# Performance work log

Hardware: AMD Instinct MI355X
Metric: run time of the kernel (lower is better)

The kernel has to match this reference:

```python
import jax, jax.numpy as jnp
import numpy as np

NUM_HEADS = 16

def _apply_rope(x, cos, sin):
    # x: (B, H, T, D); cos/sin: (T, D//2)
    B, H, T, D = x.shape
    xr = x.reshape(B, H, T, D // 2, 2)
    x0, x1 = xr[..., 0], xr[..., 1]
    c = cos[None, None, :, :]
    s = sin[None, None, :, :]
    out = jnp.stack([x0 * c - x1 * s, x0 * s + x1 * c], axis=-1)
    return out.reshape(B, H, T, D)


def setup_inputs() -> dict:
    key = jax.random.key(0)
    k1, k2, k3 = jax.random.split(key, 3)
    B, T, C = 2, 2048, 1024
    D = C // NUM_HEADS
    x = jax.random.normal(k1, (B, T, C), dtype=jnp.float32)
    qkv_w = jax.random.normal(k2, (3 * C, C), dtype=jnp.float32) * (C ** -0.5)
    proj_w = jax.random.normal(k3, (C, C), dtype=jnp.float32) * (C ** -0.5)
    # standard RoPE frequency table (theta = 10000)
    inv_freq = 1.0 / (10000.0 ** (jnp.arange(0, D, 2, dtype=jnp.float32) / D))  # (D/2,)
    angles = jnp.arange(T, dtype=jnp.float32)[:, None] * inv_freq[None, :]      # (T, D/2)
    return {
        "x": x,
        "freqs_cos": jnp.cos(angles),
        "freqs_sin": jnp.sin(angles),
        "qkv_w": qkv_w,
        "proj_w": proj_w,
    }


def reference(x, freqs_cos, freqs_sin, qkv_w, proj_w):
    B, T, C = x.shape
    H = NUM_HEADS
    D = C // H
    qkv = x @ qkv_w.T                                  # (B, T, 3C)
    q, k, v = jnp.split(qkv, 3, axis=-1)
    q = q.reshape(B, T, H, D).transpose(0, 2, 1, 3)    # (B, H, T, D)
    k = k.reshape(B, T, H, D).transpose(0, 2, 1, 3)
    v = v.reshape(B, T, H, D).transpose(0, 2, 1, 3)
    q = _apply_rope(q, freqs_cos, freqs_sin)
    k = _apply_rope(k, freqs_cos, freqs_sin)
    scale = 1.0 / jnp.sqrt(jnp.asarray(D, dtype=x.dtype))
    scores = jnp.einsum('bhqd,bhkd->bhqk', q, k) * scale
    causal = jnp.tril(jnp.ones((T, T), dtype=bool))
    scores = jnp.where(causal[None, None], scores, jnp.finfo(scores.dtype).min)
    attn = jax.nn.softmax(scores, axis=-1)
    out = jnp.einsum('bhqk,bhkd->bhqd', attn, v)       # (B, H, T, D)
    out = out.transpose(0, 2, 1, 3).reshape(B, T, C)
    return out @ proj_w.T
```

## Files before the change

### kernel.cpp

```cpp
#include <hip/hip_runtime.h>
#include <stdint.h>

#define DI __device__ __forceinline__

typedef unsigned short u16;
typedef __bf16 bf16x8 __attribute__((ext_vector_type(8)));
typedef unsigned short u16x8 __attribute__((ext_vector_type(8)));
typedef unsigned short u16x4 __attribute__((ext_vector_type(4)));
typedef float f32x4 __attribute__((ext_vector_type(4)));

DI u16 f2bf(float f) { __bf16 h = (__bf16)f; return __builtin_bit_cast(u16, h); }
DI float bf2f(u16 u) { return (float)__builtin_bit_cast(__bf16, u); }

DI bf16x8 ld8(const u16* p) { return __builtin_bit_cast(bf16x8, *(const u16x8*)p); }

DI f32x4 mfma16(bf16x8 a, bf16x8 b, f32x4 c) {
  return __builtin_amdgcn_mfma_f32_16x16x32_bf16(a, b, c, 0, 0, 0);
}

DI void async16(const u16* g, u16* l) {
  __builtin_amdgcn_global_load_lds((const __attribute__((address_space(1))) void*)g,
                                   (__attribute__((address_space(3))) void*)l, 16, 0, 0);
}

__global__ __launch_bounds__(256) void cast_bf16_k(const float* __restrict__ in,
                                                   u16* __restrict__ out) {
  const int i = blockIdx.x * 256 + threadIdx.x;
  const float4 v = ((const float4*)in)[i];
  u16x4 o = {f2bf(v.x), f2bf(v.y), f2bf(v.z), f2bf(v.w)};
  ((u16x4*)out)[i] = o;
}

template <int OUT_BF16>
__global__ __launch_bounds__(256) void gemm_bt(const u16* __restrict__ A,
                                               const u16* __restrict__ W,
                                               void* __restrict__ outp,
                                               int M, int N, int K) {
  __shared__ u16 sA[128 * 32];
  __shared__ u16 sB[128 * 32];
  const int tid = threadIdx.x;
  const int w = tid >> 6, L = tid & 63;
  const int lo = L & 15, quad = L >> 4;
  const int nb = N >> 7;
  const int bm = blockIdx.x / nb, bn = blockIdx.x - bm * nb;
  const int m0 = bm << 7, n0 = bn << 7;
  const int wm = (w >> 1) << 6, wn = (w & 1) << 6;

  f32x4 acc[4][4];
#pragma unroll
  for (int i = 0; i < 4; ++i)
#pragma unroll
    for (int j = 0; j < 4; ++j) acc[i][j] = 0.f;

  const int r0 = tid >> 2, s0 = tid & 3;
  const int c0 = s0 ^ ((r0 >> 1) & 3);
  const int r1 = r0 + 64;
  const int c1 = s0 ^ ((r1 >> 1) & 3);
  const size_t aRow0 = (size_t)(m0 + r0) * K, aRow1 = (size_t)(m0 + r1) * K;
  const size_t bRow0 = (size_t)(n0 + r0) * K, bRow1 = (size_t)(n0 + r1) * K;

  int raf[4], rbf[4];
#pragma unroll
  for (int mt = 0; mt < 4; ++mt) {
    int r = wm + mt * 16 + lo;
    raf[mt] = r * 32 + ((quad ^ ((r >> 1) & 3)) << 3);
    r = wn + mt * 16 + lo;
    rbf[mt] = r * 32 + ((quad ^ ((r >> 1) & 3)) << 3);
  }

  const int kIters = K >> 5;
  for (int kt = 0; kt < kIters; ++kt) {
    const int kb = kt << 5;
    async16(A + aRow0 + kb + c0 * 8, &sA[tid * 8]);
    async16(A + aRow1 + kb + c1 * 8, &sA[(tid + 256) * 8]);
    async16(W + bRow0 + kb + c0 * 8, &sB[tid * 8]);
    async16(W + bRow1 + kb + c1 * 8, &sB[(tid + 256) * 8]);
    __syncthreads();
    bf16x8 af[4], bfr[4];
#pragma unroll
    for (int mt = 0; mt < 4; ++mt) af[mt] = ld8(&sA[raf[mt]]);
#pragma unroll
    for (int nt = 0; nt < 4; ++nt) bfr[nt] = ld8(&sB[rbf[nt]]);
#pragma unroll
    for (int mt = 0; mt < 4; ++mt)
#pragma unroll
      for (int nt = 0; nt < 4; ++nt)
        acc[mt][nt] = mfma16(af[mt], bfr[nt], acc[mt][nt]);
    __syncthreads();
  }

#pragma unroll
  for (int mt = 0; mt < 4; ++mt) {
    const int m = m0 + wm + mt * 16 + quad * 4;
#pragma unroll
    for (int nt = 0; nt < 4; ++nt) {
      const int n = n0 + wn + nt * 16 + lo;
#pragma unroll
      for (int r = 0; r < 4; ++r) {
        const size_t off = (size_t)(m + r) * N + n;
        if (OUT_BF16)
          ((u16*)outp)[off] = f2bf(acc[mt][nt][r]);
        else
          ((float*)outp)[off] = acc[mt][nt][r];
      }
    }
  }
}

__global__ __launch_bounds__(256) void rope_k(const u16* __restrict__ qkv,
                                              const float* __restrict__ cosb,
                                              const float* __restrict__ sinb,
                                              u16* __restrict__ qo, u16* __restrict__ ko,
                                              u16* __restrict__ vo) {
  const int idx = blockIdx.x * 256 + threadIdx.x;
  const int i = idx & 31;
  const int t = (idx >> 5) & 2047;
  const int h = (idx >> 16) & 15;
  const int b = idx >> 20;
  const size_t src = ((size_t)(b * 2048 + t)) * 3072 + h * 64 + 2 * i;
  const float q0v = bf2f(qkv[src]), q1v = bf2f(qkv[src + 1]);
  const float k0v = bf2f(qkv[src + 1024]), k1v = bf2f(qkv[src + 1025]);
  const float c = cosb[t * 32 + i], s = sinb[t * 32 + i];
  const size_t dst = ((size_t)((b * 16 + h) * 2048 + t)) * 64 + 2 * i;
  qo[dst] = f2bf((q0v * c - q1v * s) * 0.125f);
  qo[dst + 1] = f2bf((q0v * s + q1v * c) * 0.125f);
  ko[dst] = f2bf(k0v * c - k1v * s);
  ko[dst + 1] = f2bf(k0v * s + k1v * c);
  vo[dst] = qkv[src + 2048];
  vo[dst + 1] = qkv[src + 2049];
}

__global__ __launch_bounds__(256) void fattn(const u16* __restrict__ qs,
                                             const u16* __restrict__ ks,
                                             const u16* __restrict__ vs,
                                             u16* __restrict__ aout) {
  __shared__ u16 sK[64 * 64];
  __shared__ u16 sVt[64 * 64];
  __shared__ u16 sP[4][32 * 64];
  const int tid = threadIdx.x;
  const int w = tid >> 6, L = tid & 63;
  const int lo = L & 15, quad = L >> 4;
  const int bh = blockIdx.x & 31;
  const int qi = 15 - (blockIdx.x >> 5);
  const size_t hoff = (size_t)bh * (2048 * 64);
  const int q0 = qi << 7;
  const int wq = q0 + w * 32;
  u16* sPw = sP[w];

  bf16x8 qb[2][2];
#pragma unroll
  for (int nt = 0; nt < 2; ++nt)
#pragma unroll
    for (int kd = 0; kd < 2; ++kd)
      qb[nt][kd] = ld8(qs + hoff + (size_t)(wq + nt * 16 + lo) * 64 + kd * 32 + quad * 8);

  float m_s[2] = {-3.0e38f, -3.0e38f};
  float l_s[2] = {0.f, 0.f};
  f32x4 ot[4][2];
#pragma unroll
  for (int mt = 0; mt < 4; ++mt) {
    ot[mt][0] = 0.f;
    ot[mt][1] = 0.f;
  }

  const int ntiles = (q0 + 128) >> 6;
  for (int kt = 0; kt < ntiles; ++kt) {
    const int kv0 = kt << 6;
#pragma unroll
    for (int it = 0; it < 2; ++it) {
      const int id = tid + it * 256;
      const int kv = id >> 3, s = id & 7, c = s ^ (kv & 7);
      async16(ks + hoff + (size_t)(kv0 + kv) * 64 + c * 8, &sK[id * 8]);
    }
#pragma unroll
    for (int it = 0; it < 2; ++it) {
      const int id = tid + it * 256;
      const int kv = id & 63, cd = id >> 6;
      u16x8 v8 = *(const u16x8*)(vs + hoff + (size_t)(kv0 + kv) * 64 + cd * 8);
#pragma unroll
      for (int j = 0; j < 8; ++j) {
        const int d = cd * 8 + j;
        sVt[d * 64 + (((kv >> 3) ^ (d & 7)) << 3) + (kv & 7)] = v8[j];
      }
    }
    __syncthreads();
    if (kv0 <= wq + 31) {
      f32x4 st[4][2];
#pragma unroll
      for (int mt = 0; mt < 4; ++mt) {
        st[mt][0] = 0.f;
        st[mt][1] = 0.f;
      }
#pragma unroll
      for (int mt = 0; mt < 4; ++mt) {
        const int kv = mt * 16 + lo;
#pragma unroll
        for (int kd = 0; kd < 2; ++kd) {
          const int c = kd * 4 + quad;
          bf16x8 ka = ld8(&sK[kv * 64 + ((c ^ (kv & 7)) << 3)]);
          st[mt][0] = mfma16(ka, qb[0][kd], st[mt][0]);
          st[mt][1] = mfma16(ka, qb[1][kd], st[mt][1]);
        }
      }
      if (kv0 + 63 > wq) {
#pragma unroll
        for (int mt = 0; mt < 4; ++mt)
#pragma unroll
          for (int nt = 0; nt < 2; ++nt)
#pragma unroll
            for (int r = 0; r < 4; ++r) {
              const int kvg = kv0 + mt * 16 + quad * 4 + r;
              const int qg = wq + nt * 16 + lo;
              if (kvg > qg) st[mt][nt][r] = -3.0e38f;
            }
      }
      float alpha[2];
#pragma unroll
      for (int nt = 0; nt < 2; ++nt) {
        float mx = -3.0e38f;
#pragma unroll
        for (int mt = 0; mt < 4; ++mt)
#pragma unroll
          for (int r = 0; r < 4; ++r) mx = fmaxf(mx, st[mt][nt][r]);
        mx = fmaxf(mx, __shfl_xor(mx, 16));
        mx = fmaxf(mx, __shfl_xor(mx, 32));
        const float mnew = fmaxf(m_s[nt], mx);
        alpha[nt] = __expf(m_s[nt] - mnew);
        float rs = 0.f;
#pragma unroll
        for (int mt = 0; mt < 4; ++mt)
#pragma unroll
          for (int r = 0; r < 4; ++r) {
            float p = __expf(st[mt][nt][r] - mnew);
            p = bf2f(f2bf(p));
            st[mt][nt][r] = p;
            rs += p;
          }
        rs += __shfl_xor(rs, 16);
        rs += __shfl_xor(rs, 32);
        l_s[nt] = l_s[nt] * alpha[nt] + rs;
        m_s[nt] = mnew;
      }
#pragma unroll
      for (int mt = 0; mt < 4; ++mt)
#pragma unroll
        for (int nt = 0; nt < 2; ++nt) {
          u16x4 pk = {f2bf(st[mt][nt][0]), f2bf(st[mt][nt][1]), f2bf(st[mt][nt][2]),
                      f2bf(st[mt][nt][3])};
          const int q = nt * 16 + lo;
          const int c2 = 2 * mt + (quad >> 1);
          *(u16x4*)&sPw[q * 64 + ((c2 ^ (q & 7)) << 3) + (quad & 1) * 4] = pk;
        }
#pragma unroll
      for (int mt = 0; mt < 4; ++mt)
#pragma unroll
        for (int nt = 0; nt < 2; ++nt)
#pragma unroll
          for (int r = 0; r < 4; ++r) ot[mt][nt][r] *= alpha[nt];
      asm volatile("s_waitcnt lgkmcnt(0)" ::: "memory");
      bf16x8 pbf[2][2];
#pragma unroll
      for (int nt = 0; nt < 2; ++nt)
#pragma unroll
        for (int kh = 0; kh < 2; ++kh) {
          const int q = nt * 16 + lo;
          const int c = kh * 4 + quad;
          pbf[nt][kh] = ld8(&sPw[q * 64 + ((c ^ (q & 7)) << 3)]);
        }
#pragma unroll
      for (int mt = 0; mt < 4; ++mt) {
        const int d = mt * 16 + lo;
#pragma unroll
        for (int kh = 0; kh < 2; ++kh) {
          const int c = kh * 4 + quad;
          bf16x8 va = ld8(&sVt[d * 64 + ((c ^ (d & 7)) << 3)]);
          ot[mt][0] = mfma16(va, pbf[0][kh], ot[mt][0]);
          ot[mt][1] = mfma16(va, pbf[1][kh], ot[mt][1]);
        }
      }
    }
    __syncthreads();
  }

  const float inv0 = 1.f / l_s[0], inv1 = 1.f / l_s[1];
#pragma unroll
  for (int mt = 0; mt < 4; ++mt)
#pragma unroll
    for (int nt = 0; nt < 2; ++nt) {
      const float iv = nt ? inv1 : inv0;
      u16x4 ok = {f2bf(ot[mt][nt][0] * iv), f2bf(ot[mt][nt][1] * iv),
                  f2bf(ot[mt][nt][2] * iv), f2bf(ot[mt][nt][3] * iv)};
      const int q = nt * 16 + lo;
      const int c2 = 2 * mt + (quad >> 1);
      *(u16x4*)&sPw[q * 64 + ((c2 ^ (q & 7)) << 3) + (quad & 1) * 4] = ok;
    }
  asm volatile("s_waitcnt lgkmcnt(0)" ::: "memory");
  const int b = bh >> 4, h = bh & 15;
#pragma unroll
  for (int rr = 0; rr < 4; ++rr) {
    const int q = rr * 8 + (L >> 3);
    const int cd = L & 7;
    u16x8 o8 = *(const u16x8*)&sPw[q * 64 + ((cd ^ (q & 7)) << 3)];
    const int t = wq + q;
    *(u16x8*)(aout + ((size_t)(b * 2048 + t)) * 1024 + h * 64 + cd * 8) = o8;
  }
}

extern "C" void kernel_launch(void* const* d_in, const int* in_sizes, int n_in,
                              void* d_out, int out_size, void* d_ws, size_t ws_size,
                              hipStream_t stream) {
  const float* x = (const float*)d_in[0];
  const float* fcos = (const float*)d_in[1];
  const float* fsin = (const float*)d_in[2];
  const float* qkvw = (const float*)d_in[3];
  const float* projw = (const float*)d_in[4];
  float* out = (float*)d_out;

  char* ws = (char*)d_ws;
  u16* x_bf = (u16*)(ws);
  u16* qkvw_bf = (u16*)(ws + (8u << 20));
  u16* projw_bf = (u16*)(ws + (14u << 20));
  u16* qkv_bf = (u16*)(ws + (16u << 20));
  u16* q_bf = (u16*)(ws + (40u << 20));
  u16* k_bf = (u16*)(ws + (48u << 20));
  u16* v_bf = (u16*)(ws + (56u << 20));
  u16* attn_bf = (u16*)(ws + (64u << 20));

  cast_bf16_k<<<4096, 256, 0, stream>>>(x, x_bf);
  cast_bf16_k<<<3072, 256, 0, stream>>>(qkvw, qkvw_bf);
  cast_bf16_k<<<1024, 256, 0, stream>>>(projw, projw_bf);
  gemm_bt<1><<<768, 256, 0, stream>>>(x_bf, qkvw_bf, (void*)qkv_bf, 4096, 3072, 1024);
  rope_k<<<8192, 256, 0, stream>>>(qkv_bf, fcos, fsin, q_bf, k_bf, v_bf);
  fattn<<<512, 256, 0, stream>>>(q_bf, k_bf, v_bf, attn_bf);
  gemm_bt<0><<<256, 256, 0, stream>>>(attn_bf, projw_bf, (void*)out, 4096, 1024, 1024);
}
```

Before: 222.9 us.

## Pre-transpose V in a separate kernel and shrink attention query tiles to 64

```diff
diff --git a/kernel.cpp b/kernel.cpp
--- a/kernel.cpp
+++ b/kernel.cpp
@@ -110,8 +110,7 @@
 __global__ __launch_bounds__(256) void rope_k(const u16* __restrict__ qkv,
                                               const float* __restrict__ cosb,
                                               const float* __restrict__ sinb,
-                                              u16* __restrict__ qo, u16* __restrict__ ko,
-                                              u16* __restrict__ vo) {
+                                              u16* __restrict__ qo, u16* __restrict__ ko) {
   const int idx = blockIdx.x * 256 + threadIdx.x;
   const int i = idx & 31;
   const int t = (idx >> 5) & 2047;
@@ -126,44 +125,64 @@
   qo[dst + 1] = f2bf((q0v * s + q1v * c) * 0.125f);
   ko[dst] = f2bf(k0v * c - k1v * s);
   ko[dst + 1] = f2bf(k0v * s + k1v * c);
-  vo[dst] = qkv[src + 2048];
-  vo[dst + 1] = qkv[src + 2049];
+}
+
+__global__ __launch_bounds__(256) void vt_k(const u16* __restrict__ qkv,
+                                            u16* __restrict__ vt) {
+  __shared__ u16 sT[64 * 64];
+  const int tid = threadIdx.x;
+  const int bh = blockIdx.x & 31;
+  const int t0 = (blockIdx.x >> 5) << 6;
+  const int b = bh >> 4, h = bh & 15;
+#pragma unroll
+  for (int it = 0; it < 2; ++it) {
+    const int id = tid + it * 256;
+    const int tr = id >> 3, s = id & 7, c = s ^ (tr & 7);
+    async16(qkv + (size_t)(b * 2048 + t0 + tr) * 3072 + 2048 + h * 64 + c * 8, &sT[id * 8]);
+  }
+  __syncthreads();
+#pragma unroll
+  for (int it = 0; it < 2; ++it) {
+    const int id = tid + it * 256;
+    const int d = id >> 3, ct = id & 7;
+    u16x8 o;
+#pragma unroll
+    for (int j = 0; j < 8; ++j) {
+      const int t = ct * 8 + j;
+      o[j] = sT[t * 64 + (((d >> 3) ^ (t & 7)) << 3) + (d & 7)];
+    }
+    *(u16x8*)(vt + ((size_t)bh * 64 + d) * 2048 + t0 + ct * 8) = o;
+  }
 }
 
 __global__ __launch_bounds__(256) void fattn(const u16* __restrict__ qs,
                                              const u16* __restrict__ ks,
-                                             const u16* __restrict__ vs,
+                                             const u16* __restrict__ vt,
                                              u16* __restrict__ aout) {
   __shared__ u16 sK[64 * 64];
   __shared__ u16 sVt[64 * 64];
-  __shared__ u16 sP[4][32 * 64];
+  __shared__ u16 sP[4][16 * 64];
   const int tid = threadIdx.x;
   const int w = tid >> 6, L = tid & 63;
   const int lo = L & 15, quad = L >> 4;
   const int bh = blockIdx.x & 31;
-  const int qi = 15 - (blockIdx.x >> 5);
+  const int qi = 31 - (blockIdx.x >> 5);
   const size_t hoff = (size_t)bh * (2048 * 64);
-  const int q0 = qi << 7;
-  const int wq = q0 + w * 32;
+  const int q0 = qi << 6;
+  const int wq = q0 + w * 16;
   u16* sPw = sP[w];
 
-  bf16x8 qb[2][2];
-#pragma unroll
-  for (int nt = 0; nt < 2; ++nt)
-#pragma unroll
-    for (int kd = 0; kd < 2; ++kd)
-      qb[nt][kd] = ld8(qs + hoff + (size_t)(wq + nt * 16 + lo) * 64 + kd * 32 + quad * 8);
-
-  float m_s[2] = {-3.0e38f, -3.0e38f};
-  float l_s[2] = {0.f, 0.f};
-  f32x4 ot[4][2];
-#pragma unroll
-  for (int mt = 0; mt < 4; ++mt) {
-    ot[mt][0] = 0.f;
-    ot[mt][1] = 0.f;
-  }
-
-  const int ntiles = (q0 + 128) >> 6;
+  bf16x8 qb[2];
+#pragma unroll
+  for (int kd = 0; kd < 2; ++kd)
+    qb[kd] = ld8(qs + hoff + (size_t)(wq + lo) * 64 + kd * 32 + quad * 8);
+
+  float m_s = -3.0e38f, l_s = 0.f;
+  f32x4 ot[4];
+#pragma unroll
+  for (int mt = 0; mt < 4; ++mt) ot[mt] = 0.f;
+
+  const int ntiles = qi + 1;
   for (int kt = 0; kt < ntiles; ++kt) {
     const int kv0 = kt << 6;
 #pragma unroll
@@ -175,129 +194,99 @@
 #pragma unroll
     for (int it = 0; it < 2; ++it) {
       const int id = tid + it * 256;
-      const int kv = id & 63, cd = id >> 6;
-      u16x8 v8 = *(const u16x8*)(vs + hoff + (size_t)(kv0 + kv) * 64 + cd * 8);
-#pragma unroll
-      for (int j = 0; j < 8; ++j) {
-        const int d = cd * 8 + j;
-        sVt[d * 64 + (((kv >> 3) ^ (d & 7)) << 3) + (kv & 7)] = v8[j];
+      const int d = id >> 3, s = id & 7, c = s ^ (d & 7);
+      async16(vt + hoff + (size_t)d * 2048 + kv0 + c * 8, &sVt[id * 8]);
+    }
+    __syncthreads();
+
+    f32x4 st[4];
+#pragma unroll
+    for (int mt = 0; mt < 4; ++mt) st[mt] = 0.f;
+#pragma unroll
+    for (int mt = 0; mt < 4; ++mt) {
+      const int kv = mt * 16 + lo;
+#pragma unroll
+      for (int kd = 0; kd < 2; ++kd) {
+        const int c = kd * 4 + quad;
+        bf16x8 ka = ld8(&sK[kv * 64 + ((c ^ (kv & 7)) << 3)]);
+        st[mt] = mfma16(ka, qb[kd], st[mt]);
       }
     }
+    if (kt == qi) {
+      const int qg = wq + lo;
+#pragma unroll
+      for (int mt = 0; mt < 4; ++mt)
+#pragma unroll
+        for (int r = 0; r < 4; ++r) {
+          const int kvg = kv0 + mt * 16 + quad * 4 + r;
+          if (kvg > qg) st[mt][r] = -3.0e38f;
+        }
+    }
+    float mx = -3.0e38f;
+#pragma unroll
+    for (int mt = 0; mt < 4; ++mt)
+#pragma unroll
+      for (int r = 0; r < 4; ++r) mx = fmaxf(mx, st[mt][r]);
+    mx = fmaxf(mx, __shfl_xor(mx, 16));
+    mx = fmaxf(mx, __shfl_xor(mx, 32));
+    const float mnew = fmaxf(m_s, mx);
+    const float alpha = __expf(m_s - mnew);
+    float rs = 0.f;
+#pragma unroll
+    for (int mt = 0; mt < 4; ++mt)
+#pragma unroll
+      for (int r = 0; r < 4; ++r) {
+        float p = __expf(st[mt][r] - mnew);
+        p = bf2f(f2bf(p));
+        st[mt][r] = p;
+        rs += p;
+      }
+    rs += __shfl_xor(rs, 16);
+    rs += __shfl_xor(rs, 32);
+    l_s = l_s * alpha + rs;
+    m_s = mnew;
+#pragma unroll
+    for (int mt = 0; mt < 4; ++mt) {
+      u16x4 pk = {f2bf(st[mt][0]), f2bf(st[mt][1]), f2bf(st[mt][2]), f2bf(st[mt][3])};
+      const int c2 = 2 * mt + (quad >> 1);
+      *(u16x4*)&sPw[lo * 64 + ((c2 ^ (lo & 7)) << 3) + (quad & 1) * 4] = pk;
+    }
+#pragma unroll
+    for (int mt = 0; mt < 4; ++mt)
+#pragma unroll
+      for (int r = 0; r < 4; ++r) ot[mt][r] *= alpha;
+    asm volatile("s_waitcnt lgkmcnt(0)" ::: "memory");
+    bf16x8 pbf[2];
+#pragma unroll
+    for (int kh = 0; kh < 2; ++kh) {
+      const int c = kh * 4 + quad;
+      pbf[kh] = ld8(&sPw[lo * 64 + ((c ^ (lo & 7)) << 3)]);
+    }
+#pragma unroll
+    for (int mt = 0; mt < 4; ++mt) {
+      const int d = mt * 16 + lo;
+#pragma unroll
+      for (int kh = 0; kh < 2; ++kh) {
+        const int c = kh * 4 + quad;
+        bf16x8 va = ld8(&sVt[d * 64 + ((c ^ (d & 7)) << 3)]);
+        ot[mt] = mfma16(va, pbf[kh], ot[mt]);
+      }
+    }
     __syncthreads();
-    if (kv0 <= wq + 31) {
-      f32x4 st[4][2];
-#pragma unroll
-      for (int mt = 0; mt < 4; ++mt) {
-        st[mt][0] = 0.f;
-        st[mt][1] = 0.f;
-      }
-#pragma unroll
-      for (int mt = 0; mt < 4; ++mt) {
-        const int kv = mt * 16 + lo;
-#pragma unroll
-        for (int kd = 0; kd < 2; ++kd) {
-          const int c = kd * 4 + quad;
-          bf16x8 ka = ld8(&sK[kv * 64 + ((c ^ (kv & 7)) << 3)]);
-          st[mt][0] = mfma16(ka, qb[0][kd], st[mt][0]);
-          st[mt][1] = mfma16(ka, qb[1][kd], st[mt][1]);
-        }
-      }
-      if (kv0 + 63 > wq) {
-#pragma unroll
-        for (int mt = 0; mt < 4; ++mt)
-#pragma unroll
-          for (int nt = 0; nt < 2; ++nt)
-#pragma unroll
-            for (int r = 0; r < 4; ++r) {
-              const int kvg = kv0 + mt * 16 + quad * 4 + r;
-              const int qg = wq + nt * 16 + lo;
-              if (kvg > qg) st[mt][nt][r] = -3.0e38f;
-            }
-      }
-      float alpha[2];
-#pragma unroll
-      for (int nt = 0; nt < 2; ++nt) {
-        float mx = -3.0e38f;
-#pragma unroll
-        for (int mt = 0; mt < 4; ++mt)
-#pragma unroll
-          for (int r = 0; r < 4; ++r) mx = fmaxf(mx, st[mt][nt][r]);
-        mx = fmaxf(mx, __shfl_xor(mx, 16));
-        mx = fmaxf(mx, __shfl_xor(mx, 32));
-        const float mnew = fmaxf(m_s[nt], mx);
-        alpha[nt] = __expf(m_s[nt] - mnew);
-        float rs = 0.f;
-#pragma unroll
-        for (int mt = 0; mt < 4; ++mt)
-#pragma unroll
-          for (int r = 0; r < 4; ++r) {
-            float p = __expf(st[mt][nt][r] - mnew);
-            p = bf2f(f2bf(p));
-            st[mt][nt][r] = p;
-            rs += p;
-          }
-        rs += __shfl_xor(rs, 16);
-        rs += __shfl_xor(rs, 32);
-        l_s[nt] = l_s[nt] * alpha[nt] + rs;
-        m_s[nt] = mnew;
-      }
-#pragma unroll
-      for (int mt = 0; mt < 4; ++mt)
-#pragma unroll
-        for (int nt = 0; nt < 2; ++nt) {
-          u16x4 pk = {f2bf(st[mt][nt][0]), f2bf(st[mt][nt][1]), f2bf(st[mt][nt][2]),
-                      f2bf(st[mt][nt][3])};
-          const int q = nt * 16 + lo;
-          const int c2 = 2 * mt + (quad >> 1);
-          *(u16x4*)&sPw[q * 64 + ((c2 ^ (q & 7)) << 3) + (quad & 1) * 4] = pk;
-        }
-#pragma unroll
-      for (int mt = 0; mt < 4; ++mt)
-#pragma unroll
-        for (int nt = 0; nt < 2; ++nt)
-#pragma unroll
-          for (int r = 0; r < 4; ++r) ot[mt][nt][r] *= alpha[nt];
-      asm volatile("s_waitcnt lgkmcnt(0)" ::: "memory");
-      bf16x8 pbf[2][2];
-#pragma unroll
-      for (int nt = 0; nt < 2; ++nt)
-#pragma unroll
-        for (int kh = 0; kh < 2; ++kh) {
-          const int q = nt * 16 + lo;
-          const int c = kh * 4 + quad;
-          pbf[nt][kh] = ld8(&sPw[q * 64 + ((c ^ (q & 7)) << 3)]);
-        }
-#pragma unroll
-      for (int mt = 0; mt < 4; ++mt) {
-        const int d = mt * 16 + lo;
-#pragma unroll
-        for (int kh = 0; kh < 2; ++kh) {
-          const int c = kh * 4 + quad;
-          bf16x8 va = ld8(&sVt[d * 64 + ((c ^ (d & 7)) << 3)]);
-          ot[mt][0] = mfma16(va, pbf[0][kh], ot[mt][0]);
-          ot[mt][1] = mfma16(va, pbf[1][kh], ot[mt][1]);
-        }
-      }
-    }
-    __syncthreads();
-  }
-
-  const float inv0 = 1.f / l_s[0], inv1 = 1.f / l_s[1];
-#pragma unroll
-  for (int mt = 0; mt < 4; ++mt)
-#pragma unroll
-    for (int nt = 0; nt < 2; ++nt) {
-      const float iv = nt ? inv1 : inv0;
-      u16x4 ok = {f2bf(ot[mt][nt][0] * iv), f2bf(ot[mt][nt][1] * iv),
-                  f2bf(ot[mt][nt][2] * iv), f2bf(ot[mt][nt][3] * iv)};
-      const int q = nt * 16 + lo;
-      const int c2 = 2 * mt + (quad >> 1);
-      *(u16x4*)&sPw[q * 64 + ((c2 ^ (q & 7)) << 3) + (quad & 1) * 4] = ok;
-    }
+  }
+
+  const float iv = 1.f / l_s;
+#pragma unroll
+  for (int mt = 0; mt < 4; ++mt) {
+    u16x4 ok = {f2bf(ot[mt][0] * iv), f2bf(ot[mt][1] * iv), f2bf(ot[mt][2] * iv),
+                f2bf(ot[mt][3] * iv)};
+    const int c2 = 2 * mt + (quad >> 1);
+    *(u16x4*)&sPw[lo * 64 + ((c2 ^ (lo & 7)) << 3) + (quad & 1) * 4] = ok;
+  }
   asm volatile("s_waitcnt lgkmcnt(0)" ::: "memory");
   const int b = bh >> 4, h = bh & 15;
 #pragma unroll
-  for (int rr = 0; rr < 4; ++rr) {
+  for (int rr = 0; rr < 2; ++rr) {
     const int q = rr * 8 + (L >> 3);
     const int cd = L & 7;
     u16x8 o8 = *(const u16x8*)&sPw[q * 64 + ((cd ^ (q & 7)) << 3)];
@@ -323,14 +312,15 @@
   u16* qkv_bf = (u16*)(ws + (16u << 20));
   u16* q_bf = (u16*)(ws + (40u << 20));
   u16* k_bf = (u16*)(ws + (48u << 20));
-  u16* v_bf = (u16*)(ws + (56u << 20));
+  u16* vt = (u16*)(ws + (56u << 20));
   u16* attn_bf = (u16*)(ws + (64u << 20));
 
   cast_bf16_k<<<4096, 256, 0, stream>>>(x, x_bf);
   cast_bf16_k<<<3072, 256, 0, stream>>>(qkvw, qkvw_bf);
   cast_bf16_k<<<1024, 256, 0, stream>>>(projw, projw_bf);
   gemm_bt<1><<<768, 256, 0, stream>>>(x_bf, qkvw_bf, (void*)qkv_bf, 4096, 3072, 1024);
-  rope_k<<<8192, 256, 0, stream>>>(qkv_bf, fcos, fsin, q_bf, k_bf, v_bf);
-  fattn<<<512, 256, 0, stream>>>(q_bf, k_bf, v_bf, attn_bf);
+  rope_k<<<8192, 256, 0, stream>>>(qkv_bf, fcos, fsin, q_bf, k_bf);
+  vt_k<<<1024, 256, 0, stream>>>(qkv_bf, vt);
+  fattn<<<1024, 256, 0, stream>>>(q_bf, k_bf, vt, attn_bf);
   gemm_bt<0><<<256, 256, 0, stream>>>(attn_bf, projw_bf, (void*)out, 4096, 1024, 1024);
 }
```

Result: faster. 204.7 us (-8.2%).
